# Performance work log

Hardware: AMD Instinct MI355X
Metric: run time of the kernel (lower is better)

The kernel has to match this reference:

```python
import jax, jax.numpy as jnp
import numpy as np

H = 8            # num_heads
DK = 256         # head_qk_dim
DV = 512         # head_v_dim
EPS = 1e-5
ROPE_BASE = 10000.0


def _rope(x):
    # x: [B, T, H, DK]; GPT-NeoX style (non-interleaved halves), seqlen_offset=0
    B, T, h, d = x.shape
    inv_freq = 1.0 / (ROPE_BASE ** (jnp.arange(0, d, 2, dtype=jnp.float32) / d))  # [d/2]
    t = jnp.arange(T, dtype=jnp.float32)
    freqs = t[:, None] * inv_freq[None, :]              # [T, d/2]
    cos = jnp.cos(freqs)[None, :, None, :]              # [1, T, 1, d/2]
    sin = jnp.sin(freqs)[None, :, None, :]
    x1, x2 = x[..., : d // 2], x[..., d // 2 :]
    return jnp.concatenate([x1 * cos - x2 * sin, x2 * cos + x1 * sin], axis=-1)


def setup_inputs() -> dict:
    key = jax.random.key(0)
    ks = jax.random.split(key, 7)
    hidden = 2048
    B, T = 2, 2048
    w = 0.02
    return {
        "hidden_states": jax.random.normal(ks[0], (B, T, hidden), jnp.float32),
        "Wq": jax.random.normal(ks[1], (hidden, H * DK), jnp.float32) * w,
        "Wk": jax.random.normal(ks[2], (hidden, H * DK), jnp.float32) * w,
        "Wv": jax.random.normal(ks[3], (hidden, H * DV), jnp.float32) * w,
        "Wg": jax.random.normal(ks[4], (hidden, H * DV), jnp.float32) * w,
        "Wo": jax.random.normal(ks[5], (H * DV, hidden), jnp.float32) * w,
        "g_norm_weight": jnp.ones((DV,), jnp.float32),
    }


def reference(hidden_states, Wq, Wk, Wv, Wg, Wo, g_norm_weight):
    B, T, _ = hidden_states.shape
    q = (hidden_states @ Wq).reshape(B, T, H, DK)
    k = (hidden_states @ Wk).reshape(B, T, H, DK)
    v = (hidden_states @ Wv).reshape(B, T, H, DV)
    g = (hidden_states @ Wg).reshape(B, T, H, DV)

    q = _rope(q)
    k = _rope(k)

    # per-head RetNet decay: gamma_h = 1 - 2^(-5-h)
    gamma = 1.0 - jnp.exp2(-5.0 - jnp.arange(H, dtype=jnp.float32))     # [H]
    idx = jnp.arange(T)
    diff = idx[:, None] - idx[None, :]                                   # [T, T]
    causal = diff >= 0
    log2g = jnp.log2(gamma)[:, None, None]                               # [H,1,1]
    D = jnp.where(causal[None], jnp.exp2(log2g * jnp.where(causal, diff, 0)[None]), 0.0)  # [H,T,T]

    scale = DK ** -0.5
    scores = jnp.einsum("bihd,bjhd->bhij", q * scale, k) * D[None]       # [B,H,T,T]
    o = jnp.einsum("bhij,bjhd->bihd", scores, v)                          # [B,T,H,DV]

    # fused RMSNorm (per head over DV) + swish gate
    rms = jax.lax.rsqrt(jnp.mean(o * o, axis=-1, keepdims=True) + EPS)
    o = o * rms * g_norm_weight
    o = o * (g * jax.nn.sigmoid(g))

    return o.reshape(B, T, H * DV) @ Wo
```

## Files before the change

kernel.cpp:

```cpp
#include <hip/hip_runtime.h>
#include <hip/hip_bf16.h>
#include <math.h>

#define NH 8
#define DKk 256
#define DVv 512
#define Bn 2
#define Tn 2048
#define HID 2048
#define EPSf 1e-5f

typedef __bf16 bf16x8 __attribute__((ext_vector_type(8)));
typedef float f32x4 __attribute__((ext_vector_type(4)));
typedef unsigned short us8 __attribute__((ext_vector_type(8)));
using bf16 = __hip_bfloat16;
typedef unsigned short ushort_t;

__device__ __forceinline__ void gload_lds16(const void* g, void* lds_base) {
  __builtin_amdgcn_global_load_lds(
      (const __attribute__((address_space(1))) void*)g,
      (__attribute__((address_space(3))) void*)lds_base, 16, 0, 0);
}

__device__ __forceinline__ ushort_t f2bf_raw(float f) {
  bf16 h = __float2bfloat16(f);
  return *reinterpret_cast<ushort_t*>(&h);
}
__device__ __forceinline__ float bf2f_raw(ushort_t u) {
  union { unsigned int i; float f; } v; v.i = ((unsigned int)u) << 16; return v.f;
}

__global__ void k_f32_to_bf16(const float4* __restrict__ in, ushort4* __restrict__ out, int n4) {
  int i = blockIdx.x * blockDim.x + threadIdx.x;
  if (i >= n4) return;
  float4 v = in[i];
  ushort4 o;
  o.x = f2bf_raw(v.x); o.y = f2bf_raw(v.y); o.z = f2bf_raw(v.z); o.w = f2bf_raw(v.w);
  out[i] = o;
}

__global__ void k_transpose_w(const float* __restrict__ W, bf16* __restrict__ WT, int K, int N) {
  __shared__ float t[32][33];
  int n0 = blockIdx.x * 32, k0 = blockIdx.y * 32;
  int tx = threadIdx.x, ty = threadIdx.y;
#pragma unroll
  for (int i = 0; i < 4; i++)
    t[ty + i * 8][tx] = W[(size_t)(k0 + ty + i * 8) * N + n0 + tx];
  __syncthreads();
#pragma unroll
  for (int i = 0; i < 4; i++)
    WT[(size_t)(n0 + ty + i * 8) * K + k0 + tx] = __float2bfloat16(t[tx][ty + i * 8]);
}

__global__ void k_build_vS(const ushort_t* __restrict__ v, ushort_t* __restrict__ vS) {
  __shared__ ushort_t t[32 * 520];
  const int tid = threadIdx.x;
  const int kt = blockIdx.x;
  const int bh = blockIdx.y;
  const int b = bh >> 3, h = bh & 7;
#pragma unroll
  for (int r = 0; r < 8; r++) {
    int j = r * 4 + (tid >> 6);
    int vec = tid & 63;
    us8 d = *(const us8*)(v + (((size_t)(b * Tn + kt * 32 + j) * NH + h) * DVv) + vec * 8);
    *(us8*)(&t[j * 520 + vec * 8]) = d;
  }
  __syncthreads();
#pragma unroll
  for (int u = 0; u < 8; u++) {
    int uid = u * 256 + tid;
    int chunk = uid >> 9;
    int dv = uid & 511;
    us8 o;
#pragma unroll
    for (int jj = 0; jj < 8; jj++) o[jj] = t[(chunk * 8 + jj) * 520 + dv];
    *(us8*)(vS + ((size_t)(bh * 64 + kt) * 2048 + chunk * 512 + dv) * 8) = o;
  }
}

__global__ void k_rope(bf16* __restrict__ x, float scale) {
  int tid = blockIdx.x * 256 + threadIdx.x;
  int i = tid & 127;
  int h = (tid >> 7) & 7;
  int t = (tid >> 10) & (Tn - 1);
  int b = tid >> 21;
  float inv = exp2f(-(float)i * (13.287712379549449f / 128.0f));
  float ang = (float)t * inv;
  float s, c;
  sincosf(ang, &s, &c);
  size_t base = ((size_t)(b * Tn + t) * NH + h) * DKk + i;
  float x1 = __bfloat162float(x[base]);
  float x2 = __bfloat162float(x[base + 128]);
  x[base]       = __float2bfloat16((x1 * c - x2 * s) * scale);
  x[base + 128] = __float2bfloat16((x2 * c + x1 * s) * scale);
}

template <bool OUT_BF16>
__global__ __launch_bounds__(256) void k_gemm(const bf16* __restrict__ A, const bf16* __restrict__ BT,
                                              void* __restrict__ Cout, int M, int N, int K) {
  __shared__ __align__(16) bf16 a_lds[128 * 32];
  __shared__ __align__(16) bf16 b_lds[128 * 32];
  const int tid = threadIdx.x;
  const int l = tid & 63;
  const int w = tid >> 6;
  const int wr = w >> 1, wc = w & 1;
  const int m0 = blockIdx.y * 128, n0 = blockIdx.x * 128;
  const int quad = l >> 4, c16 = l & 15;

  const int lrow = l >> 2;
  const int loff = (l & 3) * 16;
  const char* aG0 = (const char*)(A + (size_t)(m0 + w * 32 + lrow) * K) + loff;
  const char* aG1 = (const char*)(A + (size_t)(m0 + w * 32 + 16 + lrow) * K) + loff;
  const char* bG0 = (const char*)(BT + (size_t)(n0 + w * 32 + lrow) * K) + loff;
  const char* bG1 = (const char*)(BT + (size_t)(n0 + w * 32 + 16 + lrow) * K) + loff;
  char* aL0 = (char*)a_lds + w * 2048;
  char* aL1 = (char*)a_lds + w * 2048 + 1024;
  char* bL0 = (char*)b_lds + w * 2048;
  char* bL1 = (char*)b_lds + w * 2048 + 1024;

  f32x4 acc[4][4];
  const f32x4 fz = {0.f, 0.f, 0.f, 0.f};
#pragma unroll
  for (int r = 0; r < 4; r++)
#pragma unroll
    for (int c = 0; c < 4; c++) acc[r][c] = fz;

  for (int k0 = 0; k0 < K; k0 += 32) {
    __syncthreads();
    size_t kb = (size_t)k0 * 2;
    gload_lds16(aG0 + kb, aL0);
    gload_lds16(aG1 + kb, aL1);
    gload_lds16(bG0 + kb, bL0);
    gload_lds16(bG1 + kb, bL1);
    __syncthreads();
    bf16x8 af[4], bfv[4];
#pragma unroll
    for (int r = 0; r < 4; r++)
      af[r] = *(const bf16x8*)(a_lds + (wr * 64 + r * 16 + c16) * 32 + quad * 8);
#pragma unroll
    for (int c = 0; c < 4; c++)
      bfv[c] = *(const bf16x8*)(b_lds + (wc * 64 + c * 16 + c16) * 32 + quad * 8);
#pragma unroll
    for (int r = 0; r < 4; r++)
#pragma unroll
      for (int c = 0; c < 4; c++)
        acc[r][c] = __builtin_amdgcn_mfma_f32_16x16x32_bf16(af[r], bfv[c], acc[r][c], 0, 0, 0);
  }

#pragma unroll
  for (int r = 0; r < 4; r++)
#pragma unroll
    for (int c = 0; c < 4; c++)
#pragma unroll
      for (int rr = 0; rr < 4; rr++) {
        int m = m0 + wr * 64 + r * 16 + quad * 4 + rr;
        int n = n0 + wc * 64 + c * 16 + c16;
        float val = acc[r][c][rr];
        if (OUT_BF16) ((bf16*)Cout)[(size_t)m * N + n] = __float2bfloat16(val);
        else          ((float*)Cout)[(size_t)m * N + n] = val;
      }
}

#define BARX() asm volatile("s_barrier" ::: "memory")
#define LGKM0() { asm volatile("s_waitcnt lgkmcnt(0)" ::: "memory"); __builtin_amdgcn_sched_barrier(0); }
#define VMW4() asm volatile("s_waitcnt vmcnt(4)" ::: "memory")
#define VMW0() asm volatile("s_waitcnt vmcnt(0)" ::: "memory")
#define PRIO1 __builtin_amdgcn_s_setprio(1)
#define PRIO0 __builtin_amdgcn_s_setprio(0)

#define QUADQ(MB, NB)                                                              \
  { _Pragma("unroll") for (int kk_ = 0; kk_ < 2; ++kk_)                            \
    _Pragma("unroll") for (int mf_ = 0; mf_ < 4; ++mf_)                            \
    _Pragma("unroll") for (int nf_ = 0; nf_ < 2; ++nf_)                            \
      acc[(MB) + mf_][(NB) + nf_] = __builtin_amdgcn_mfma_f32_16x16x32_bf16(       \
          ar[(MB) + mf_][kk_], br[(NB) + nf_][kk_],                                \
          acc[(MB) + mf_][(NB) + nf_], 0, 0, 0); }

__global__ __launch_bounds__(512, 2) void k_gemm8(const bf16* __restrict__ A, const bf16* __restrict__ BT,
                                                  bf16* __restrict__ O0, bf16* __restrict__ O1,
                                                  int nsplit, int M, int Ntot, int K) {
  extern __shared__ char lds[];
  const int tid = threadIdx.x;
  const int lane = tid & 63;
  const int w = tid >> 6;
  const int wr = w >> 2;
  const int wc = w & 3;
  const int quad = lane >> 4, c16 = lane & 15;
  const int m0 = blockIdx.y * 256, n0 = blockIdx.x * 256;

  const int srow = (w << 4) | (lane >> 3);
  const int gsw = (((lane & 7) ^ (lane >> 3)) << 4);
  const size_t rowBytes = (size_t)K * 2;
  const char* aS = (const char*)(A + (size_t)(m0 + srow) * K) + gsw;
  const char* bS = (const char*)(BT + (size_t)(n0 + srow) * K) + gsw;

  auto stage = [&](int matB, int buf, int h, int t) {
    const char* base = (matB ? bS : aS) + (size_t)h * 128 * rowBytes + (size_t)t * 128;
    char* ldst = lds + buf * 65536 + matB * 32768 + h * 16384 + w * 2048;
    gload_lds16(base, ldst);
    gload_lds16(base + 8 * rowBytes, ldst + 1024);
  };
  auto ldA = [&](int buf, int mf, int kk) -> bf16x8 {
    int row = wr * 128 + mf * 16 + c16;
    return *(const bf16x8*)(lds + buf * 65536 + row * 128 + ((((kk << 2) | quad) ^ (c16 & 7)) << 4));
  };
  auto ldB = [&](int buf, int nf, int kk) -> bf16x8 {
    int row = wc * 64 + nf * 16 + c16;
    return *(const bf16x8*)(lds + buf * 65536 + 32768 + row * 128 + ((((kk << 2) | quad) ^ (c16 & 7)) << 4));
  };

  f32x4 acc[8][4];
  const f32x4 fz = {0.f, 0.f, 0.f, 0.f};
#pragma unroll
  for (int i = 0; i < 8; i++)
#pragma unroll
    for (int j = 0; j < 4; j++) acc[i][j] = fz;
  bf16x8 ar[8][2], br[4][2];

  const int nT = K >> 6;
  const int nIter = nT >> 1;

  stage(0, 0, 0, 0); stage(0, 0, 1, 0);
  stage(1, 0, 0, 0); stage(1, 0, 1, 0);
  stage(0, 1, 0, 1); stage(0, 1, 1, 1);
  VMW4();
  BARX();

  for (int it = 0; it < nIter; ++it) {
    const int t = it * 2;
    const bool last = (it == nIter - 1);
#pragma unroll
    for (int mf = 0; mf < 4; ++mf) { ar[mf][0] = ldA(0, mf, 0); ar[mf][1] = ldA(0, mf, 1); }
#pragma unroll
    for (int nf = 0; nf < 2; ++nf) { br[nf][0] = ldB(0, nf, 0); br[nf][1] = ldB(0, nf, 1); }
    stage(1, 1, 0, t + 1);
    BARX(); LGKM0();
    PRIO1; QUADQ(0, 0); PRIO0;
    BARX();
#pragma unroll
    for (int mf = 4; mf < 8; ++mf) { ar[mf][0] = ldA(0, mf, 0); ar[mf][1] = ldA(0, mf, 1); }
    stage(1, 1, 1, t + 1);
    BARX(); LGKM0();
    PRIO1; QUADQ(4, 0); PRIO0;
    BARX();
#pragma unroll
    for (int nf = 2; nf < 4; ++nf) { br[nf][0] = ldB(0, nf, 0); br[nf][1] = ldB(0, nf, 1); }
    if (!last) stage(0, 0, 0, t + 2);
    BARX(); LGKM0();
    PRIO1; QUADQ(0, 2); PRIO0;
    BARX();
    if (!last) stage(0, 0, 1, t + 2);
    BARX();
    PRIO1; QUADQ(4, 2); PRIO0;
    if (!last) { VMW4(); } else { VMW0(); }
    BARX();
#pragma unroll
    for (int mf = 0; mf < 4; ++mf) { ar[mf][0] = ldA(1, mf, 0); ar[mf][1] = ldA(1, mf, 1); }
#pragma unroll
    for (int nf = 0; nf < 2; ++nf) { br[nf][0] = ldB(1, nf, 0); br[nf][1] = ldB(1, nf, 1); }
    if (!last) stage(1, 0, 0, t + 2);
    BARX(); LGKM0();
    PRIO1; QUADQ(0, 0); PRIO0;
    BARX();
#pragma unroll
    for (int mf = 4; mf < 8; ++mf) { ar[mf][0] = ldA(1, mf, 0); ar[mf][1] = ldA(1, mf, 1); }
    if (!last) stage(1, 0, 1, t + 2);
    BARX(); LGKM0();
    PRIO1; QUADQ(4, 0); PRIO0;
    BARX();
#pragma unroll
    for (int nf = 2; nf < 4; ++nf) { br[nf][0] = ldB(1, nf, 0); br[nf][1] = ldB(1, nf, 1); }
    if (!last) stage(0, 1, 0, t + 3);
    BARX(); LGKM0();
    PRIO1; QUADQ(0, 2); PRIO0;
    BARX();
    if (!last) stage(0, 1, 1, t + 3);
    BARX();
    PRIO1; QUADQ(4, 2); PRIO0;
    if (!last) VMW4();
    BARX();
  }

  bf16* Ob; int ldo, nc0;
  if (n0 < nsplit) { Ob = O0; ldo = nsplit; nc0 = n0; }
  else             { Ob = O1; ldo = Ntot - nsplit; nc0 = n0 - nsplit; }
#pragma unroll
  for (int mf = 0; mf < 8; ++mf)
#pragma unroll
    for (int nf = 0; nf < 4; ++nf)
#pragma unroll
      for (int rr = 0; rr < 4; ++rr) {
        int m = m0 + wr * 128 + mf * 16 + quad * 4 + rr;
        int n = nc0 + wc * 64 + nf * 16 + c16;
        Ob[(size_t)m * ldo + n] = __float2bfloat16(acc[mf][nf][rr]);
      }
}

__global__ __launch_bounds__(256, 2) void k_retention(const bf16* __restrict__ q, const bf16* __restrict__ k,
                                                      const char* __restrict__ vS, const bf16* __restrict__ g,
                                                      const float* __restrict__ gnw, bf16* __restrict__ X) {
  extern __shared__ char smem[];
  float* red = (float*)(smem + 75776);
  bf16* o_lds = (bf16*)smem;

  const int tid = threadIdx.x;
  const int l = tid & 63, w = tid >> 6;
  const int quad = l >> 4, c16 = l & 15;

  const int bid = blockIdx.x;
  const int u = (bid & 255) >> 4;
  const int qt = (bid < 256) ? (31 - u) : u;
  const int bh = bid & 15;
  const int b = bh >> 3, h = bh & 7;
  const int q0 = qt * 64;

  bf16x8 qf[8];
  {
    const bf16* qrow = q + ((size_t)(b * Tn + q0 + w * 16 + c16) * NH + h) * DKk + quad * 8;
#pragma unroll
    for (int c = 0; c < 8; c++) qf[c] = *(const bf16x8*)(qrow + c * 32);
  }

  const float log2g = log2f(1.0f - exp2f(-5.0f - (float)h));

  f32x4 acc[4][8];
  const f32x4 fz = {0.f, 0.f, 0.f, 0.f};
#pragma unroll
  for (int rt = 0; rt < 4; rt++)
#pragma unroll
    for (int n = 0; n < 8; n++) acc[rt][n] = fz;

  const int ktmax = 2 * qt + 1;
  const float Dcut = 30.0f / (-log2g);
  int kt0 = (int)fmaxf(0.0f, floorf(((float)q0 - Dcut) * (1.0f / 32.0f)));

  const char* vS_tilebase = vS + (size_t)(bh * 64) * 32768;

  auto stageK = [&](int kt) {
    const int pb = (kt - kt0) & 1;
#pragma unroll
    for (int i = 0; i < 4; i++) {
      int instr = w * 4 + i;
      int j = instr * 2 + (l >> 5);
      int cg = (l & 31) ^ (j & 7);
      const char* gp = (const char*)(k + ((size_t)(b * Tn + kt * 32 + j) * NH + h) * DKk) + cg * 16;
      gload_lds16(gp, smem + pb * 16384 + instr * 1024);
    }
  };
  auto stageV = [&](int kt) {
#pragma unroll
    for (int i = 0; i < 8; i++) {
      int instr = w * 8 + i;
      const char* gp = vS_tilebase + (size_t)kt * 32768 + instr * 1024 + l * 16;
      gload_lds16(gp, smem + 32768 + instr * 1024);
    }
  };

  auto S_phase = [&](int kt) {
    const int pb = (kt - kt0) & 1;
    f32x4 sacc[2] = {fz, fz};
#pragma unroll
    for (int jt = 0; jt < 2; jt++)
#pragma unroll
      for (int c = 0; c < 8; c++) {
        const char* kp = smem + pb * 16384 + (jt * 16 + c16) * 512 + (((c * 4 + quad) ^ (c16 & 7)) * 16);
        bf16x8 bfrag = *(const bf16x8*)kp;
        sacc[jt] = __builtin_amdgcn_mfma_f32_16x16x32_bf16(qf[c], bfrag, sacc[jt], 0, 0, 0);
      }
    ushort_t* pbuf = (ushort_t*)(smem + 65536 + pb * 5120);
#pragma unroll
    for (int jt = 0; jt < 2; jt++)
#pragma unroll
      for (int r = 0; r < 4; r++) {
        int ig = q0 + w * 16 + quad * 4 + r;
        int jg = kt * 32 + jt * 16 + c16;
        int d = ig - jg;
        float val = (d >= 0) ? sacc[jt][r] * exp2f(log2g * (float)d) : 0.0f;
        pbuf[(w * 16 + quad * 4 + r) * 40 + jt * 16 + c16] = f2bf_raw(val);
      }
  };

  auto PV_phase = [&](int kt) {
    const int pb = (kt - kt0) & 1;
    const char* pbuf = smem + 65536 + pb * 5120;
    bf16x8 pa[4];
#pragma unroll
    for (int rt = 0; rt < 4; rt++)
      pa[rt] = *(const bf16x8*)(pbuf + (rt * 16 + c16) * 80 + quad * 16);
    const char* v_lds = smem + 32768;
#pragma unroll
    for (int n = 0; n < 8; n++) {
      bf16x8 bv = *(const bf16x8*)(v_lds + quad * 8192 + (w * 128 + n * 16 + c16) * 16);
#pragma unroll
      for (int rt = 0; rt < 4; rt++)
        acc[rt][n] = __builtin_amdgcn_mfma_f32_16x16x32_bf16(pa[rt], bv, acc[rt][n], 0, 0, 0);
    }
  };

#define SBAR() { __builtin_amdgcn_sched_barrier(0); __builtin_amdgcn_s_barrier(); }
#define WLGKM0() { asm volatile("s_waitcnt lgkmcnt(0)" ::: "memory"); }

  stageK(kt0);
  stageV(kt0);
  asm volatile("s_waitcnt vmcnt(8)" ::: "memory");
  SBAR();
  S_phase(kt0);
  if (kt0 + 1 <= ktmax) stageK(kt0 + 1);
  WLGKM0(); SBAR();

  for (int kt = kt0 + 1; kt <= ktmax; ++kt) {
    asm volatile("s_waitcnt vmcnt(4)" ::: "memory");
    SBAR();
    PV_phase(kt - 1);
    WLGKM0(); SBAR();
    stageV(kt);
    asm volatile("s_waitcnt vmcnt(8)" ::: "memory");
    SBAR();
    S_phase(kt);
    if (kt + 1 <= ktmax) stageK(kt + 1);
    WLGKM0(); SBAR();
  }

  asm volatile("s_waitcnt vmcnt(0)" ::: "memory");
  SBAR();
  PV_phase(ktmax);

  __syncthreads();
#pragma unroll
  for (int rt = 0; rt < 4; rt++)
#pragma unroll
    for (int r = 0; r < 4; r++) {
      float s = 0.f;
#pragma unroll
      for (int n = 0; n < 8; n++) { float v = acc[rt][n][r]; s += v * v; }
      s += __shfl_xor(s, 1);
      s += __shfl_xor(s, 2);
      s += __shfl_xor(s, 4);
      s += __shfl_xor(s, 8);
      if (c16 == 0) red[(rt * 16 + quad * 4 + r) * 4 + w] = s;
    }
  __syncthreads();
  float ss[4][4];
#pragma unroll
  for (int rt = 0; rt < 4; rt++)
#pragma unroll
    for (int r = 0; r < 4; r++) {
      int row = rt * 16 + quad * 4 + r;
      float tot = red[row * 4] + red[row * 4 + 1] + red[row * 4 + 2] + red[row * 4 + 3];
      ss[rt][r] = rsqrtf(tot * (1.0f / DVv) + EPSf);
    }
  __syncthreads();

#pragma unroll
  for (int n = 0; n < 8; n++) {
    int col = w * 128 + n * 16 + c16;
    float gw = gnw[col];
#pragma unroll
    for (int rt = 0; rt < 4; rt++)
#pragma unroll
      for (int r = 0; r < 4; r++) {
        int row = rt * 16 + quad * 4 + r;
        o_lds[row * 512 + col] = __float2bfloat16(acc[rt][n][r] * ss[rt][r] * gw);
      }
  }
  __syncthreads();

#pragma unroll
  for (int it = 0; it < 16; it++) {
    int cid = it * 256 + tid;
    int row = cid >> 6;
    int cp = (cid & 63) * 8;
    const ushort_t* gp = (const ushort_t*)g + ((size_t)(b * Tn + q0 + row) * NH + h) * DVv + cp;
    us8 gv = *(const us8*)gp;
    us8 ov;
#pragma unroll
    for (int e = 0; e < 8; e++) {
      float gf = bf2f_raw(gv[e]);
      float gate = gf / (1.0f + expf(-gf));
      float of = __bfloat162float(o_lds[row * 512 + cp + e]);
      ov[e] = f2bf_raw(of * gate);
    }
    *(us8*)((ushort_t*)X + ((size_t)(b * Tn + q0 + row) * NH + h) * DVv + cp) = ov;
  }
}

extern "C" void kernel_launch(void* const* d_in, const int* in_sizes, int n_in,
                              void* d_out, int out_size, void* d_ws, size_t ws_size,
                              hipStream_t stream) {
  const float* hs  = (const float*)d_in[0];
  const float* Wq  = (const float*)d_in[1];
  const float* Wk  = (const float*)d_in[2];
  const float* Wv  = (const float*)d_in[3];
  const float* Wg  = (const float*)d_in[4];
  const float* Wo  = (const float*)d_in[5];
  const float* gnw = (const float*)d_in[6];
  float* out = (float*)d_out;
  char* ws = (char*)d_ws;

  bf16* hsb = (bf16*)(ws);
  bf16* WqT = (bf16*)(ws + 16777216);
  bf16* WkT = (bf16*)(ws + 25165824);
  bf16* WvT = (bf16*)(ws + 33554432);
  bf16* WgT = (bf16*)(ws + 50331648);
  char* vSb = ws;
  bf16* WoT = (bf16*)(ws + 33554432);
  bf16* qb = (bf16*)(ws + 67108864);
  bf16* kb = (bf16*)(ws + 83886080);
  bf16* vb = (bf16*)(ws + 100663296);
  bf16* gb = (bf16*)(ws + 134217728);
  bf16* Xb = vb;

  static bool attr_done = false;
  if (!attr_done) {
    hipFuncSetAttribute((const void*)k_gemm8, hipFuncAttributeMaxDynamicSharedMemorySize, 131072);
    hipFuncSetAttribute((const void*)k_retention, hipFuncAttributeMaxDynamicSharedMemorySize, 76800);
    attr_done = true;
  }

  dim3 tb(32, 8);

  k_f32_to_bf16<<<8192, 256, 0, stream>>>((const float4*)hs, (ushort4*)hsb, 2097152);
  k_transpose_w<<<dim3(HID / 32, HID / 32), tb, 0, stream>>>(Wq, WqT, HID, HID);
  k_transpose_w<<<dim3(HID / 32, HID / 32), tb, 0, stream>>>(Wk, WkT, HID, HID);
  k_transpose_w<<<dim3(NH * DVv / 32, HID / 32), tb, 0, stream>>>(Wv, WvT, HID, NH * DVv);
  k_transpose_w<<<dim3(NH * DVv / 32, HID / 32), tb, 0, stream>>>(Wg, WgT, HID, NH * DVv);
  k_gemm8<<<dim3(16, 16), 512, 131072, stream>>>(hsb, WqT, qb, kb, 2048, 4096, 4096, 2048);
  k_gemm8<<<dim3(32, 16), 512, 131072, stream>>>(hsb, WvT, vb, gb, 4096, 4096, 8192, 2048);
  k_rope<<<16384, 256, 0, stream>>>(qb, 0.0625f);
  k_rope<<<16384, 256, 0, stream>>>(kb, 1.0f);
  k_build_vS<<<dim3(64, 16), 256, 0, stream>>>((const ushort_t*)vb, (ushort_t*)vSb);
  k_transpose_w<<<dim3(HID / 32, NH * DVv / 32), tb, 0, stream>>>(Wo, WoT, NH * DVv, HID);
  k_retention<<<512, 256, 76800, stream>>>(qb, kb, vSb, gb, gnw, Xb);
  k_gemm<false><<<dim3(16, 32), 256, 0, stream>>>(Xb, WoT, out, 4096, 2048, 4096);
}
```

Baseline: 621.1 us.

## Keep retention P tile in registers via shuffles and give each wave full DV rows

The retention kernel now computes S transposed (K as the A operand) and moves the decayed, masked P fragment between lanes with shuffles. This replaces the round trip through an LDS buffer and drops a barrier per tile. Each wave now owns its own 16 query rows across all 512 V columns, so the RMSNorm reduction stays inside the wave with no LDS reduction or extra syncs. The decay is factored into a per-tile exponent times per-lane precomputed constants, and LDS use shrinks to 64KB. The input-projection GEMM also issues more LDS fragment loads ahead of the partial lgkmcnt waits. The cost is that every wave reads all of V from LDS, and the per-wave accumulator tiles change shape.

```diff
diff --git a/kernel.cpp b/kernel.cpp
--- a/kernel.cpp
+++ b/kernel.cpp
@@ -13,6 +13,7 @@
 typedef __bf16 bf16x8 __attribute__((ext_vector_type(8)));
 typedef float f32x4 __attribute__((ext_vector_type(4)));
 typedef unsigned short us8 __attribute__((ext_vector_type(8)));
+typedef unsigned int u32x4 __attribute__((ext_vector_type(4)));
 using bf16 = __hip_bfloat16;
 typedef unsigned short ushort_t;
 
@@ -163,10 +164,13 @@
 
 #define BARX() asm volatile("s_barrier" ::: "memory")
 #define LGKM0() { asm volatile("s_waitcnt lgkmcnt(0)" ::: "memory"); __builtin_amdgcn_sched_barrier(0); }
+#define LGKM8() { asm volatile("s_waitcnt lgkmcnt(8)" ::: "memory"); __builtin_amdgcn_sched_barrier(0); }
+#define LGKM4() { asm volatile("s_waitcnt lgkmcnt(4)" ::: "memory"); __builtin_amdgcn_sched_barrier(0); }
 #define VMW4() asm volatile("s_waitcnt vmcnt(4)" ::: "memory")
 #define VMW0() asm volatile("s_waitcnt vmcnt(0)" ::: "memory")
 #define PRIO1 __builtin_amdgcn_s_setprio(1)
 #define PRIO0 __builtin_amdgcn_s_setprio(0)
+#define SCHEDB() __builtin_amdgcn_sched_barrier(0)
 
 #define QUADQ(MB, NB)                                                              \
   { _Pragma("unroll") for (int kk_ = 0; kk_ < 2; ++kk_)                            \
@@ -233,18 +237,19 @@
     for (int mf = 0; mf < 4; ++mf) { ar[mf][0] = ldA(0, mf, 0); ar[mf][1] = ldA(0, mf, 1); }
 #pragma unroll
     for (int nf = 0; nf < 2; ++nf) { br[nf][0] = ldB(0, nf, 0); br[nf][1] = ldB(0, nf, 1); }
+    SCHEDB();
+#pragma unroll
+    for (int mf = 4; mf < 8; ++mf) { ar[mf][0] = ldA(0, mf, 0); ar[mf][1] = ldA(0, mf, 1); }
     stage(1, 1, 0, t + 1);
-    BARX(); LGKM0();
+    BARX(); LGKM8();
     PRIO1; QUADQ(0, 0); PRIO0;
     BARX();
 #pragma unroll
-    for (int mf = 4; mf < 8; ++mf) { ar[mf][0] = ldA(0, mf, 0); ar[mf][1] = ldA(0, mf, 1); }
+    for (int nf = 2; nf < 4; ++nf) { br[nf][0] = ldB(0, nf, 0); br[nf][1] = ldB(0, nf, 1); }
     stage(1, 1, 1, t + 1);
-    BARX(); LGKM0();
+    BARX(); LGKM4();
     PRIO1; QUADQ(4, 0); PRIO0;
     BARX();
-#pragma unroll
-    for (int nf = 2; nf < 4; ++nf) { br[nf][0] = ldB(0, nf, 0); br[nf][1] = ldB(0, nf, 1); }
     if (!last) stage(0, 0, 0, t + 2);
     BARX(); LGKM0();
     PRIO1; QUADQ(0, 2); PRIO0;
@@ -258,18 +263,19 @@
     for (int mf = 0; mf < 4; ++mf) { ar[mf][0] = ldA(1, mf, 0); ar[mf][1] = ldA(1, mf, 1); }
 #pragma unroll
     for (int nf = 0; nf < 2; ++nf) { br[nf][0] = ldB(1, nf, 0); br[nf][1] = ldB(1, nf, 1); }
+    SCHEDB();
+#pragma unroll
+    for (int mf = 4; mf < 8; ++mf) { ar[mf][0] = ldA(1, mf, 0); ar[mf][1] = ldA(1, mf, 1); }
     if (!last) stage(1, 0, 0, t + 2);
-    BARX(); LGKM0();
+    BARX(); LGKM8();
     PRIO1; QUADQ(0, 0); PRIO0;
     BARX();
 #pragma unroll
-    for (int mf = 4; mf < 8; ++mf) { ar[mf][0] = ldA(1, mf, 0); ar[mf][1] = ldA(1, mf, 1); }
+    for (int nf = 2; nf < 4; ++nf) { br[nf][0] = ldB(1, nf, 0); br[nf][1] = ldB(1, nf, 1); }
     if (!last) stage(1, 0, 1, t + 2);
-    BARX(); LGKM0();
+    BARX(); LGKM4();
     PRIO1; QUADQ(4, 0); PRIO0;
     BARX();
-#pragma unroll
-    for (int nf = 2; nf < 4; ++nf) { br[nf][0] = ldB(1, nf, 0); br[nf][1] = ldB(1, nf, 1); }
     if (!last) stage(0, 1, 0, t + 3);
     BARX(); LGKM0();
     PRIO1; QUADQ(0, 2); PRIO0;
@@ -296,11 +302,12 @@
       }
 }
 
+#define SBARR() { __builtin_amdgcn_sched_barrier(0); __builtin_amdgcn_s_barrier(); }
+
 __global__ __launch_bounds__(256, 2) void k_retention(const bf16* __restrict__ q, const bf16* __restrict__ k,
                                                       const char* __restrict__ vS, const bf16* __restrict__ g,
                                                       const float* __restrict__ gnw, bf16* __restrict__ X) {
   extern __shared__ char smem[];
-  float* red = (float*)(smem + 75776);
   bf16* o_lds = (bf16*)smem;
 
   const int tid = threadIdx.x;
@@ -323,12 +330,17 @@
 
   const float log2g = log2f(1.0f - exp2f(-5.0f - (float)h));
 
-  f32x4 acc[4][8];
+  float cinv[2][4];
+#pragma unroll
+  for (int jt = 0; jt < 2; jt++)
+#pragma unroll
+    for (int r = 0; r < 4; r++)
+      cinv[jt][r] = exp2f(-log2g * (float)(jt * 16 + quad * 4 + r));
+
+  f32x4 acc[32];
   const f32x4 fz = {0.f, 0.f, 0.f, 0.f};
 #pragma unroll
-  for (int rt = 0; rt < 4; rt++)
-#pragma unroll
-    for (int n = 0; n < 8; n++) acc[rt][n] = fz;
+  for (int n = 0; n < 32; n++) acc[n] = fz;
 
   const int ktmax = 2 * qt + 1;
   const float Dcut = 30.0f / (-log2g);
@@ -356,7 +368,7 @@
     }
   };
 
-  auto S_phase = [&](int kt) {
+  auto S_phase = [&](int kt) -> bf16x8 {
     const int pb = (kt - kt0) & 1;
     f32x4 sacc[2] = {fz, fz};
 #pragma unroll
@@ -364,104 +376,88 @@
 #pragma unroll
       for (int c = 0; c < 8; c++) {
         const char* kp = smem + pb * 16384 + (jt * 16 + c16) * 512 + (((c * 4 + quad) ^ (c16 & 7)) * 16);
-        bf16x8 bfrag = *(const bf16x8*)kp;
-        sacc[jt] = __builtin_amdgcn_mfma_f32_16x16x32_bf16(qf[c], bfrag, sacc[jt], 0, 0, 0);
+        bf16x8 kfrag = *(const bf16x8*)kp;
+        sacc[jt] = __builtin_amdgcn_mfma_f32_16x16x32_bf16(kfrag, qf[c], sacc[jt], 0, 0, 0);
       }
-    ushort_t* pbuf = (ushort_t*)(smem + 65536 + pb * 5120);
+    const int base = (q0 + w * 16 + c16) - kt * 32;
+    const float tb = exp2f(log2g * (float)base);
+    unsigned int pk[2][2];
 #pragma unroll
     for (int jt = 0; jt < 2; jt++)
 #pragma unroll
-      for (int r = 0; r < 4; r++) {
-        int ig = q0 + w * 16 + quad * 4 + r;
-        int jg = kt * 32 + jt * 16 + c16;
-        int d = ig - jg;
-        float val = (d >= 0) ? sacc[jt][r] * exp2f(log2g * (float)d) : 0.0f;
-        pbuf[(w * 16 + quad * 4 + r) * 40 + jt * 16 + c16] = f2bf_raw(val);
+      for (int s = 0; s < 2; s++) {
+        int off0 = jt * 16 + quad * 4 + 2 * s;
+        float v0 = (base >= off0)     ? sacc[jt][2 * s]     * tb * cinv[jt][2 * s]     : 0.0f;
+        float v1 = (base >= off0 + 1) ? sacc[jt][2 * s + 1] * tb * cinv[jt][2 * s + 1] : 0.0f;
+        pk[jt][s] = (unsigned int)f2bf_raw(v0) | ((unsigned int)f2bf_raw(v1) << 16);
       }
-  };
-
-  auto PV_phase = [&](int kt) {
-    const int pb = (kt - kt0) & 1;
-    const char* pbuf = smem + 65536 + pb * 5120;
-    bf16x8 pa[4];
-#pragma unroll
-    for (int rt = 0; rt < 4; rt++)
-      pa[rt] = *(const bf16x8*)(pbuf + (rt * 16 + c16) * 80 + quad * 16);
+    u32x4 pu;
+#pragma unroll
+    for (int t = 0; t < 4; t++) {
+      int src = ((2 * (quad & 1) + (t >> 1)) << 4) | c16;
+      unsigned int a0 = (unsigned int)__shfl((int)pk[0][t & 1], src, 64);
+      unsigned int a1 = (unsigned int)__shfl((int)pk[1][t & 1], src, 64);
+      pu[t] = (quad < 2) ? a0 : a1;
+    }
+    return __builtin_bit_cast(bf16x8, pu);
+  };
+
+  auto PV_phase = [&](bf16x8 pa) {
     const char* v_lds = smem + 32768;
 #pragma unroll
-    for (int n = 0; n < 8; n++) {
-      bf16x8 bv = *(const bf16x8*)(v_lds + quad * 8192 + (w * 128 + n * 16 + c16) * 16);
-#pragma unroll
-      for (int rt = 0; rt < 4; rt++)
-        acc[rt][n] = __builtin_amdgcn_mfma_f32_16x16x32_bf16(pa[rt], bv, acc[rt][n], 0, 0, 0);
+    for (int n = 0; n < 32; n++) {
+      bf16x8 bv = *(const bf16x8*)(v_lds + quad * 8192 + (n * 16 + c16) * 16);
+      acc[n] = __builtin_amdgcn_mfma_f32_16x16x32_bf16(pa, bv, acc[n], 0, 0, 0);
     }
   };
-
-#define SBAR() { __builtin_amdgcn_sched_barrier(0); __builtin_amdgcn_s_barrier(); }
-#define WLGKM0() { asm volatile("s_waitcnt lgkmcnt(0)" ::: "memory"); }
 
   stageK(kt0);
   stageV(kt0);
   asm volatile("s_waitcnt vmcnt(8)" ::: "memory");
-  SBAR();
-  S_phase(kt0);
+  SBARR();
+  bf16x8 paC = S_phase(kt0);
   if (kt0 + 1 <= ktmax) stageK(kt0 + 1);
-  WLGKM0(); SBAR();
 
   for (int kt = kt0 + 1; kt <= ktmax; ++kt) {
     asm volatile("s_waitcnt vmcnt(4)" ::: "memory");
-    SBAR();
-    PV_phase(kt - 1);
-    WLGKM0(); SBAR();
+    SBARR();
+    PV_phase(paC);
+    asm volatile("s_waitcnt lgkmcnt(0)" ::: "memory");
+    SBARR();
     stageV(kt);
     asm volatile("s_waitcnt vmcnt(8)" ::: "memory");
-    SBAR();
-    S_phase(kt);
+    SBARR();
+    paC = S_phase(kt);
     if (kt + 1 <= ktmax) stageK(kt + 1);
-    WLGKM0(); SBAR();
   }
 
   asm volatile("s_waitcnt vmcnt(0)" ::: "memory");
-  SBAR();
-  PV_phase(ktmax);
+  SBARR();
+  PV_phase(paC);
+
+  float ss[4];
+#pragma unroll
+  for (int rr = 0; rr < 4; rr++) {
+    float s = 0.f;
+#pragma unroll
+    for (int n = 0; n < 32; n++) { float v = acc[n][rr]; s += v * v; }
+    s += __shfl_xor(s, 1);
+    s += __shfl_xor(s, 2);
+    s += __shfl_xor(s, 4);
+    s += __shfl_xor(s, 8);
+    ss[rr] = rsqrtf(s * (1.0f / DVv) + EPSf);
+  }
 
   __syncthreads();
 #pragma unroll
-  for (int rt = 0; rt < 4; rt++)
-#pragma unroll
-    for (int r = 0; r < 4; r++) {
-      float s = 0.f;
-#pragma unroll
-      for (int n = 0; n < 8; n++) { float v = acc[rt][n][r]; s += v * v; }
-      s += __shfl_xor(s, 1);
-      s += __shfl_xor(s, 2);
-      s += __shfl_xor(s, 4);
-      s += __shfl_xor(s, 8);
-      if (c16 == 0) red[(rt * 16 + quad * 4 + r) * 4 + w] = s;
+  for (int n = 0; n < 32; n++) {
+    int col = n * 16 + c16;
+    float gw = gnw[col];
+#pragma unroll
+    for (int rr = 0; rr < 4; rr++) {
+      int row = w * 16 + quad * 4 + rr;
+      o_lds[row * 512 + col] = __float2bfloat16(acc[n][rr] * ss[rr] * gw);
     }
-  __syncthreads();
-  float ss[4][4];
-#pragma unroll
-  for (int rt = 0; rt < 4; rt++)
-#pragma unroll
-    for (int r = 0; r < 4; r++) {
-      int row = rt * 16 + quad * 4 + r;
-      float tot = red[row * 4] + red[row * 4 + 1] + red[row * 4 + 2] + red[row * 4 + 3];
-      ss[rt][r] = rsqrtf(tot * (1.0f / DVv) + EPSf);
-    }
-  __syncthreads();
-
-#pragma unroll
-  for (int n = 0; n < 8; n++) {
-    int col = w * 128 + n * 16 + c16;
-    float gw = gnw[col];
-#pragma unroll
-    for (int rt = 0; rt < 4; rt++)
-#pragma unroll
-      for (int r = 0; r < 4; r++) {
-        int row = rt * 16 + quad * 4 + r;
-        o_lds[row * 512 + col] = __float2bfloat16(acc[rt][n][r] * ss[rt][r] * gw);
-      }
   }
   __syncthreads();
 
@@ -513,7 +509,7 @@
   static bool attr_done = false;
   if (!attr_done) {
     hipFuncSetAttribute((const void*)k_gemm8, hipFuncAttributeMaxDynamicSharedMemorySize, 131072);
-    hipFuncSetAttribute((const void*)k_retention, hipFuncAttributeMaxDynamicSharedMemorySize, 76800);
+    hipFuncSetAttribute((const void*)k_retention, hipFuncAttributeMaxDynamicSharedMemorySize, 65536);
     attr_done = true;
   }
 
@@ -530,6 +526,6 @@
   k_rope<<<16384, 256, 0, stream>>>(kb, 1.0f);
   k_build_vS<<<dim3(64, 16), 256, 0, stream>>>((const ushort_t*)vb, (ushort_t*)vSb);
   k_transpose_w<<<dim3(HID / 32, NH * DVv / 32), tb, 0, stream>>>(Wo, WoT, NH * DVv, HID);
-  k_retention<<<512, 256, 76800, stream>>>(qb, kb, vSb, gb, gnw, Xb);
+  k_retention<<<512, 256, 65536, stream>>>(qb, kb, vSb, gb, gnw, Xb);
   k_gemm<false><<<dim3(16, 32), 256, 0, stream>>>(Xb, WoT, out, 4096, 2048, 4096);
 }
```

Result: slower. 652.6 us (+5.1%).

## Use tuned 256x256 GEMM with split-K for output projection, add reduction

Applied to the files above, without the earlier changes.

Replaces the simple 128x128 output-projection GEMM with the pipelined 256x256 k_gemm8 kernel, templated to write fp32 partial results. K is split in two via blockIdx.z so the 8x16 tile grid yields 256 blocks, and a separate elementwise kernel sums the two fp32 partials into the output. This aims to raise MFMA efficiency and occupancy for the final projection, at the cost of extra fp32 partial traffic and one more launch. The workspace regions reused for the partials must not overlap live buffers (Xb and WoT).

```diff
diff --git a/kernel.cpp b/kernel.cpp
--- a/kernel.cpp
+++ b/kernel.cpp
@@ -37,6 +37,15 @@
   ushort4 o;
   o.x = f2bf_raw(v.x); o.y = f2bf_raw(v.y); o.z = f2bf_raw(v.z); o.w = f2bf_raw(v.w);
   out[i] = o;
+}
+
+__global__ void k_add2_f32(const float4* __restrict__ a, const float4* __restrict__ b,
+                           float4* __restrict__ o, int n4) {
+  int i = blockIdx.x * blockDim.x + threadIdx.x;
+  if (i >= n4) return;
+  float4 x = a[i], y = b[i];
+  float4 r; r.x = x.x + y.x; r.y = x.y + y.y; r.z = x.z + y.z; r.w = x.w + y.w;
+  o[i] = r;
 }
 
 __global__ void k_transpose_w(const float* __restrict__ W, bf16* __restrict__ WT, int K, int N) {
@@ -95,72 +104,6 @@
   x[base + 128] = __float2bfloat16((x2 * c + x1 * s) * scale);
 }
 
-template <bool OUT_BF16>
-__global__ __launch_bounds__(256) void k_gemm(const bf16* __restrict__ A, const bf16* __restrict__ BT,
-                                              void* __restrict__ Cout, int M, int N, int K) {
-  __shared__ __align__(16) bf16 a_lds[128 * 32];
-  __shared__ __align__(16) bf16 b_lds[128 * 32];
-  const int tid = threadIdx.x;
-  const int l = tid & 63;
-  const int w = tid >> 6;
-  const int wr = w >> 1, wc = w & 1;
-  const int m0 = blockIdx.y * 128, n0 = blockIdx.x * 128;
-  const int quad = l >> 4, c16 = l & 15;
-
-  const int lrow = l >> 2;
-  const int loff = (l & 3) * 16;
-  const char* aG0 = (const char*)(A + (size_t)(m0 + w * 32 + lrow) * K) + loff;
-  const char* aG1 = (const char*)(A + (size_t)(m0 + w * 32 + 16 + lrow) * K) + loff;
-  const char* bG0 = (const char*)(BT + (size_t)(n0 + w * 32 + lrow) * K) + loff;
-  const char* bG1 = (const char*)(BT + (size_t)(n0 + w * 32 + 16 + lrow) * K) + loff;
-  char* aL0 = (char*)a_lds + w * 2048;
-  char* aL1 = (char*)a_lds + w * 2048 + 1024;
-  char* bL0 = (char*)b_lds + w * 2048;
-  char* bL1 = (char*)b_lds + w * 2048 + 1024;
-
-  f32x4 acc[4][4];
-  const f32x4 fz = {0.f, 0.f, 0.f, 0.f};
-#pragma unroll
-  for (int r = 0; r < 4; r++)
-#pragma unroll
-    for (int c = 0; c < 4; c++) acc[r][c] = fz;
-
-  for (int k0 = 0; k0 < K; k0 += 32) {
-    __syncthreads();
-    size_t kb = (size_t)k0 * 2;
-    gload_lds16(aG0 + kb, aL0);
-    gload_lds16(aG1 + kb, aL1);
-    gload_lds16(bG0 + kb, bL0);
-    gload_lds16(bG1 + kb, bL1);
-    __syncthreads();
-    bf16x8 af[4], bfv[4];
-#pragma unroll
-    for (int r = 0; r < 4; r++)
-      af[r] = *(const bf16x8*)(a_lds + (wr * 64 + r * 16 + c16) * 32 + quad * 8);
-#pragma unroll
-    for (int c = 0; c < 4; c++)
-      bfv[c] = *(const bf16x8*)(b_lds + (wc * 64 + c * 16 + c16) * 32 + quad * 8);
-#pragma unroll
-    for (int r = 0; r < 4; r++)
-#pragma unroll
-      for (int c = 0; c < 4; c++)
-        acc[r][c] = __builtin_amdgcn_mfma_f32_16x16x32_bf16(af[r], bfv[c], acc[r][c], 0, 0, 0);
-  }
-
-#pragma unroll
-  for (int r = 0; r < 4; r++)
-#pragma unroll
-    for (int c = 0; c < 4; c++)
-#pragma unroll
-      for (int rr = 0; rr < 4; rr++) {
-        int m = m0 + wr * 64 + r * 16 + quad * 4 + rr;
-        int n = n0 + wc * 64 + c * 16 + c16;
-        float val = acc[r][c][rr];
-        if (OUT_BF16) ((bf16*)Cout)[(size_t)m * N + n] = __float2bfloat16(val);
-        else          ((float*)Cout)[(size_t)m * N + n] = val;
-      }
-}
-
 #define BARX() asm volatile("s_barrier" ::: "memory")
 #define LGKM0() { asm volatile("s_waitcnt lgkmcnt(0)" ::: "memory"); __builtin_amdgcn_sched_barrier(0); }
 #define VMW4() asm volatile("s_waitcnt vmcnt(4)" ::: "memory")
@@ -176,9 +119,10 @@
           ar[(MB) + mf_][kk_], br[(NB) + nf_][kk_],                                \
           acc[(MB) + mf_][(NB) + nf_], 0, 0, 0); }
 
+template <bool F32S>
 __global__ __launch_bounds__(512, 2) void k_gemm8(const bf16* __restrict__ A, const bf16* __restrict__ BT,
-                                                  bf16* __restrict__ O0, bf16* __restrict__ O1,
-                                                  int nsplit, int M, int Ntot, int K) {
+                                                  void* __restrict__ O0, void* __restrict__ O1,
+                                                  int nsplit, int M, int Ntot, int Kloop, int Kstride) {
   extern __shared__ char lds[];
   const int tid = threadIdx.x;
   const int lane = tid & 63;
@@ -187,12 +131,16 @@
   const int wc = w & 3;
   const int quad = lane >> 4, c16 = lane & 15;
   const int m0 = blockIdx.y * 256, n0 = blockIdx.x * 256;
+  const int ks = blockIdx.z;
+
+  const bf16* Ab = A + (size_t)ks * Kloop;
+  const bf16* Bb = BT + (size_t)ks * Kloop;
 
   const int srow = (w << 4) | (lane >> 3);
   const int gsw = (((lane & 7) ^ (lane >> 3)) << 4);
-  const size_t rowBytes = (size_t)K * 2;
-  const char* aS = (const char*)(A + (size_t)(m0 + srow) * K) + gsw;
-  const char* bS = (const char*)(BT + (size_t)(n0 + srow) * K) + gsw;
+  const size_t rowBytes = (size_t)Kstride * 2;
+  const char* aS = (const char*)(Ab + (size_t)(m0 + srow) * Kstride) + gsw;
+  const char* bS = (const char*)(Bb + (size_t)(n0 + srow) * Kstride) + gsw;
 
   auto stage = [&](int matB, int buf, int h, int t) {
     const char* base = (matB ? bS : aS) + (size_t)h * 128 * rowBytes + (size_t)t * 128;
@@ -217,7 +165,7 @@
     for (int j = 0; j < 4; j++) acc[i][j] = fz;
   bf16x8 ar[8][2], br[4][2];
 
-  const int nT = K >> 6;
+  const int nT = Kloop >> 6;
   const int nIter = nT >> 1;
 
   stage(0, 0, 0, 0); stage(0, 0, 1, 0);
@@ -281,25 +229,40 @@
     BARX();
   }
 
-  bf16* Ob; int ldo, nc0;
-  if (n0 < nsplit) { Ob = O0; ldo = nsplit; nc0 = n0; }
-  else             { Ob = O1; ldo = Ntot - nsplit; nc0 = n0 - nsplit; }
-#pragma unroll
-  for (int mf = 0; mf < 8; ++mf)
-#pragma unroll
-    for (int nf = 0; nf < 4; ++nf)
-#pragma unroll
-      for (int rr = 0; rr < 4; ++rr) {
-        int m = m0 + wr * 128 + mf * 16 + quad * 4 + rr;
-        int n = nc0 + wc * 64 + nf * 16 + c16;
-        Ob[(size_t)m * ldo + n] = __float2bfloat16(acc[mf][nf][rr]);
-      }
+  if (F32S) {
+    float* Ob = (float*)(ks ? O1 : O0);
+#pragma unroll
+    for (int mf = 0; mf < 8; ++mf)
+#pragma unroll
+      for (int nf = 0; nf < 4; ++nf)
+#pragma unroll
+        for (int rr = 0; rr < 4; ++rr) {
+          int m = m0 + wr * 128 + mf * 16 + quad * 4 + rr;
+          int n = n0 + wc * 64 + nf * 16 + c16;
+          Ob[(size_t)m * Ntot + n] = acc[mf][nf][rr];
+        }
+  } else {
+    bf16* Ob; int ldo, nc0;
+    if (n0 < nsplit) { Ob = (bf16*)O0; ldo = nsplit; nc0 = n0; }
+    else             { Ob = (bf16*)O1; ldo = Ntot - nsplit; nc0 = n0 - nsplit; }
+#pragma unroll
+    for (int mf = 0; mf < 8; ++mf)
+#pragma unroll
+      for (int nf = 0; nf < 4; ++nf)
+#pragma unroll
+        for (int rr = 0; rr < 4; ++rr) {
+          int m = m0 + wr * 128 + mf * 16 + quad * 4 + rr;
+          int n = nc0 + wc * 64 + nf * 16 + c16;
+          Ob[(size_t)m * ldo + n] = __float2bfloat16(acc[mf][nf][rr]);
+        }
+  }
 }
 
 __global__ __launch_bounds__(256, 2) void k_retention(const bf16* __restrict__ q, const bf16* __restrict__ k,
                                                       const char* __restrict__ vS, const bf16* __restrict__ g,
                                                       const float* __restrict__ gnw, bf16* __restrict__ X) {
   extern __shared__ char smem[];
+  ushort_t* p_lds_base = (ushort_t*)(smem + 65536);
   float* red = (float*)(smem + 75776);
   bf16* o_lds = (bf16*)smem;
 
@@ -367,7 +330,7 @@
         bf16x8 bfrag = *(const bf16x8*)kp;
         sacc[jt] = __builtin_amdgcn_mfma_f32_16x16x32_bf16(qf[c], bfrag, sacc[jt], 0, 0, 0);
       }
-    ushort_t* pbuf = (ushort_t*)(smem + 65536 + pb * 5120);
+    ushort_t* pbuf = p_lds_base + pb * 2560;
 #pragma unroll
     for (int jt = 0; jt < 2; jt++)
 #pragma unroll
@@ -382,7 +345,7 @@
 
   auto PV_phase = [&](int kt) {
     const int pb = (kt - kt0) & 1;
-    const char* pbuf = smem + 65536 + pb * 5120;
+    const char* pbuf = (const char*)(p_lds_base + pb * 2560);
     bf16x8 pa[4];
 #pragma unroll
     for (int rt = 0; rt < 4; rt++)
@@ -397,32 +360,32 @@
     }
   };
 
-#define SBAR() { __builtin_amdgcn_sched_barrier(0); __builtin_amdgcn_s_barrier(); }
+#define SBARR() { __builtin_amdgcn_sched_barrier(0); __builtin_amdgcn_s_barrier(); }
 #define WLGKM0() { asm volatile("s_waitcnt lgkmcnt(0)" ::: "memory"); }
 
   stageK(kt0);
   stageV(kt0);
   asm volatile("s_waitcnt vmcnt(8)" ::: "memory");
-  SBAR();
+  SBARR();
   S_phase(kt0);
   if (kt0 + 1 <= ktmax) stageK(kt0 + 1);
-  WLGKM0(); SBAR();
+  WLGKM0(); SBARR();
 
   for (int kt = kt0 + 1; kt <= ktmax; ++kt) {
     asm volatile("s_waitcnt vmcnt(4)" ::: "memory");
-    SBAR();
+    SBARR();
     PV_phase(kt - 1);
-    WLGKM0(); SBAR();
+    WLGKM0(); SBARR();
     stageV(kt);
     asm volatile("s_waitcnt vmcnt(8)" ::: "memory");
-    SBAR();
+    SBARR();
     S_phase(kt);
     if (kt + 1 <= ktmax) stageK(kt + 1);
-    WLGKM0(); SBAR();
+    WLGKM0(); SBARR();
   }
 
   asm volatile("s_waitcnt vmcnt(0)" ::: "memory");
-  SBAR();
+  SBARR();
   PV_phase(ktmax);
 
   __syncthreads();
@@ -509,10 +472,13 @@
   bf16* vb = (bf16*)(ws + 100663296);
   bf16* gb = (bf16*)(ws + 134217728);
   bf16* Xb = vb;
+  float* p0 = (float*)ws;
+  float* p1 = (float*)(ws + 50331648);
 
   static bool attr_done = false;
   if (!attr_done) {
-    hipFuncSetAttribute((const void*)k_gemm8, hipFuncAttributeMaxDynamicSharedMemorySize, 131072);
+    hipFuncSetAttribute((const void*)k_gemm8<false>, hipFuncAttributeMaxDynamicSharedMemorySize, 131072);
+    hipFuncSetAttribute((const void*)k_gemm8<true>, hipFuncAttributeMaxDynamicSharedMemorySize, 131072);
     hipFuncSetAttribute((const void*)k_retention, hipFuncAttributeMaxDynamicSharedMemorySize, 76800);
     attr_done = true;
   }
@@ -524,12 +490,13 @@
   k_transpose_w<<<dim3(HID / 32, HID / 32), tb, 0, stream>>>(Wk, WkT, HID, HID);
   k_transpose_w<<<dim3(NH * DVv / 32, HID / 32), tb, 0, stream>>>(Wv, WvT, HID, NH * DVv);
   k_transpose_w<<<dim3(NH * DVv / 32, HID / 32), tb, 0, stream>>>(Wg, WgT, HID, NH * DVv);
-  k_gemm8<<<dim3(16, 16), 512, 131072, stream>>>(hsb, WqT, qb, kb, 2048, 4096, 4096, 2048);
-  k_gemm8<<<dim3(32, 16), 512, 131072, stream>>>(hsb, WvT, vb, gb, 4096, 4096, 8192, 2048);
+  k_gemm8<false><<<dim3(16, 16), 512, 131072, stream>>>(hsb, WqT, qb, kb, 2048, 4096, 4096, 2048, 2048);
+  k_gemm8<false><<<dim3(32, 16), 512, 131072, stream>>>(hsb, WvT, vb, gb, 4096, 4096, 8192, 2048, 2048);
   k_rope<<<16384, 256, 0, stream>>>(qb, 0.0625f);
   k_rope<<<16384, 256, 0, stream>>>(kb, 1.0f);
   k_build_vS<<<dim3(64, 16), 256, 0, stream>>>((const ushort_t*)vb, (ushort_t*)vSb);
   k_transpose_w<<<dim3(HID / 32, NH * DVv / 32), tb, 0, stream>>>(Wo, WoT, NH * DVv, HID);
   k_retention<<<512, 256, 76800, stream>>>(qb, kb, vSb, gb, gnw, Xb);
-  k_gemm<false><<<dim3(16, 32), 256, 0, stream>>>(Xb, WoT, out, 4096, 2048, 4096);
-}
+  k_gemm8<true><<<dim3(8, 16, 2), 512, 131072, stream>>>(Xb, WoT, p0, p1, 2048, 4096, 2048, 2048, 4096);
+  k_add2_f32<<<8192, 256, 0, stream>>>((const float4*)p0, (const float4*)p1, (float4*)out, 2097152);
+}
```

Measured after the change: 600.5 us. 1.03x faster.
